# Kernel tuning notes

Measured on AMD Instinct MI355X. Metric: run time of the kernel, lower is better.

Reference implementation:

```python
import jax, jax.numpy as jnp
import numpy as np

B, T, D = 2, 2048, 1024
QH, KVH = 16, 4
HD = D // QH          # 64
G = QH // KVH         # group size 4
SCALE = HD ** -0.5


def _rope_rotate(x):
    # interleaved rotation: (x1, x2) -> (-x2, x1)
    x1 = x[..., ::2]
    x2 = x[..., 1::2]
    return jnp.stack((-x2, x1), axis=-1).reshape(x.shape)


def setup_inputs() -> dict:
    key = jax.random.key(0)
    k0, k1, k2, k3 = jax.random.split(key, 4)
    x = jax.random.normal(k0, (B, T, D), dtype=jnp.float32)
    # proper RoPE tables, shape [T, HD], each frequency repeated for the interleaved pair
    inv_freq = 1.0 / (10000.0 ** (np.arange(0, HD, 2, dtype=np.float32) / HD))
    freqs = np.arange(T, dtype=np.float32)[:, None] * inv_freq[None, :]   # [T, HD/2]
    freqs = np.repeat(freqs, 2, axis=-1)                                   # [T, HD]
    cos = jnp.asarray(np.cos(freqs), dtype=jnp.float32)
    sin = jnp.asarray(np.sin(freqs), dtype=jnp.float32)
    # glorot-uniform weights stored torch-style as [out, in]
    def glorot(k, out_d, in_d):
        lim = float(np.sqrt(6.0 / (in_d + out_d)))
        return jax.random.uniform(k, (out_d, in_d), jnp.float32, -lim, lim)
    Wq = glorot(k1, D, D)
    Wkv = glorot(k2, 2 * KVH * HD, D)
    Wo = glorot(k3, D, D)
    return {"x": x, "cos": cos, "sin": sin, "Wq": Wq, "Wkv": Wkv, "Wo": Wo}


def reference(x, cos, sin, Wq, Wkv, Wo):
    # projections (torch Linear: y = x @ W.T)
    q = (x @ Wq.T).reshape(B, T, QH, HD).transpose(0, 2, 1, 3)        # [B,QH,T,HD]
    kv = (x @ Wkv.T).reshape(B, T, KVH, 2, HD)
    k = kv[..., 0, :].transpose(0, 2, 1, 3)                            # [B,KVH,T,HD]
    v = kv[..., 1, :].transpose(0, 2, 1, 3)                            # [B,KVH,T,HD]
    # inline RoPE (cos/sin broadcast over batch & heads)
    q = q * cos + _rope_rotate(q) * sin
    k = k * cos + _rope_rotate(k) * sin
    # GQA via broadcast instead of repeat_interleave (same math)
    qg = q.reshape(B, KVH, G, T, HD)
    scores = jnp.einsum('bkgtd,bksd->bkgts', qg, k) * SCALE            # [B,KVH,G,T,T]
    attn = jax.nn.softmax(scores, axis=-1)  # dropout is identity in eval
    out = jnp.einsum('bkgts,bksd->bkgtd', attn, v)                     # [B,KVH,G,T,HD]
    out = out.reshape(B, QH, T, HD).transpose(0, 2, 1, 3).reshape(B, T, D)
    return out @ Wo.T
```

## Files before the change

kernel.cpp:

```cpp
#include <hip/hip_runtime.h>


typedef __bf16 bf16x8 __attribute__((ext_vector_type(8)));
typedef float f32x4 __attribute__((ext_vector_type(4)));
typedef float f32x16 __attribute__((ext_vector_type(16)));
typedef int i32x4 __attribute__((ext_vector_type(4)));
typedef unsigned short ushort4v __attribute__((ext_vector_type(4)));
typedef unsigned short ushort8v __attribute__((ext_vector_type(8)));
typedef unsigned short u16;
typedef unsigned int u32;

#define DEVINL __device__ __forceinline__

DEVINL float bf2f(u16 u) {
  unsigned int x = ((unsigned int)u) << 16;
  return __builtin_bit_cast(float, x);
}
DEVINL u16 f2bf(float f) {
  unsigned int x = __builtin_bit_cast(unsigned int, f);
  x += 0x7fffu + ((x >> 16) & 1u);
  return (u16)(x >> 16);
}
DEVINL float exp2r(float x) {
  float r;
  asm("v_exp_f32 %0, %1" : "=v"(r) : "v"(x));
  return r;
}

constexpr int Bb = 2, Tt = 2048, Dd = 1024, QH = 16, KVH = 4, HD = 64;
constexpr float SCALE_L2E = 0.125f * 1.44269504088896340736f;
constexpr int KVSZ = 131072;

__global__ void cvt_all(const float* __restrict__ x, const float* __restrict__ Wq,
                        const float* __restrict__ Wkv, const float* __restrict__ Wo,
                        u16* __restrict__ xb, u16* __restrict__ wqkv,
                        u16* __restrict__ wob) {
  int i = blockIdx.x * 256 + threadIdx.x;
  const float* src;
  u16* dst;
  if (i < 1048576) {
    src = x; dst = xb;
  } else if (i < 1310720) {
    src = Wq - (size_t)1048576 * 4; dst = wqkv - (size_t)1048576 * 4;
  } else if (i < 1441792) {
    src = Wkv - (size_t)1310720 * 4; dst = wqkv + (size_t)1024 * 1024 - (size_t)1310720 * 4;
  } else {
    src = Wo - (size_t)1441792 * 4; dst = wob - (size_t)1441792 * 4;
  }
  float4 v = reinterpret_cast<const float4*>(src)[i];
  ushort4v o = {f2bf(v.x), f2bf(v.y), f2bf(v.z), f2bf(v.w)};
  *reinterpret_cast<ushort4v*>(dst + (size_t)i * 4) = o;
}

template <bool OUT_F32>
__global__ __launch_bounds__(256) void gemm_bt(const u16* __restrict__ A,
                                               const u16* __restrict__ Bw,
                                               void* __restrict__ Cout, int M, int N, int K) {
  __shared__ alignas(16) u16 lA[128 * 64];
  __shared__ alignas(16) u16 lB[128 * 64];
  const int tid = threadIdx.x;
  const int w = tid >> 6, lane = tid & 63;
  const int r16 = lane & 15, g4 = lane >> 4;
  const int row0 = blockIdx.y * 128, col0 = blockIdx.x * 128;
  const int sr = tid >> 3, sc = tid & 7;
  const int NT = K >> 6;

  bf16x8 ra[4], rb[4];
  f32x4 acc[4][4];
#pragma unroll
  for (int i = 0; i < 4; ++i)
#pragma unroll
    for (int j = 0; j < 4; ++j) acc[i][j] = f32x4{0.f, 0.f, 0.f, 0.f};

  const int wm = (w >> 1) * 64, wn = (w & 1) * 64;

#pragma unroll
  for (int i = 0; i < 4; ++i) {
    int r = i * 32 + sr;
    ra[i] = *reinterpret_cast<const bf16x8*>(A + (size_t)(row0 + r) * K + sc * 8);
    rb[i] = *reinterpret_cast<const bf16x8*>(Bw + (size_t)(col0 + r) * K + sc * 8);
  }

  for (int kt = 0; kt < NT; ++kt) {
    __syncthreads();
#pragma unroll
    for (int i = 0; i < 4; ++i) {
      int r = i * 32 + sr;
      int c = (sc ^ (r & 7)) * 8;
      *reinterpret_cast<bf16x8*>(&lA[r * 64 + c]) = ra[i];
      *reinterpret_cast<bf16x8*>(&lB[r * 64 + c]) = rb[i];
    }
    __syncthreads();
    if (kt + 1 < NT) {
      int k0 = (kt + 1) << 6;
#pragma unroll
      for (int i = 0; i < 4; ++i) {
        int r = i * 32 + sr;
        ra[i] = *reinterpret_cast<const bf16x8*>(A + (size_t)(row0 + r) * K + k0 + sc * 8);
        rb[i] = *reinterpret_cast<const bf16x8*>(Bw + (size_t)(col0 + r) * K + k0 + sc * 8);
      }
    }
#pragma unroll
    for (int kk = 0; kk < 2; ++kk) {
      bf16x8 af[4], bfr[4];
#pragma unroll
      for (int mf = 0; mf < 4; ++mf) {
        int r = wm + mf * 16 + r16;
        int c = ((kk * 4 + g4) ^ (r & 7)) * 8;
        af[mf] = *reinterpret_cast<const bf16x8*>(&lA[r * 64 + c]);
      }
#pragma unroll
      for (int nf = 0; nf < 4; ++nf) {
        int r = wn + nf * 16 + r16;
        int c = ((kk * 4 + g4) ^ (r & 7)) * 8;
        bfr[nf] = *reinterpret_cast<const bf16x8*>(&lB[r * 64 + c]);
      }
#pragma unroll
      for (int mf = 0; mf < 4; ++mf)
#pragma unroll
        for (int nf = 0; nf < 4; ++nf)
          acc[mf][nf] =
              __builtin_amdgcn_mfma_f32_16x16x32_bf16(af[mf], bfr[nf], acc[mf][nf], 0, 0, 0);
    }
  }

#pragma unroll
  for (int mf = 0; mf < 4; ++mf)
#pragma unroll
    for (int nf = 0; nf < 4; ++nf)
#pragma unroll
      for (int r = 0; r < 4; ++r) {
        size_t row = (size_t)(row0 + wm + mf * 16 + g4 * 4 + r);
        size_t col = (size_t)(col0 + wn + nf * 16 + r16);
        float v = acc[mf][nf][r];
        if (OUT_F32)
          reinterpret_cast<float*>(Cout)[row * N + col] = v;
        else
          reinterpret_cast<u16*>(Cout)[row * N + col] = f2bf(v);
      }
}

__global__ void rope_scatter(const u16* __restrict__ P, const float* __restrict__ cosT,
                             const float* __restrict__ sinT, u16* __restrict__ Q,
                             u16* __restrict__ Kc) {
  int idx = blockIdx.x * 256 + threadIdx.x;
  if (idx >= (Bb * Tt) * 640) return;
  int row = idx / 640, p = idx - row * 640;
  int b = row >> 11, t = row & 2047;
  int n, d;
  u16* outp;
  float scl;
  if (p < 512) {
    n = p * 2;
    int h = n >> 6;
    d = n & 63;
    outp = Q + ((size_t)(b * QH + h) * Tt + t) * HD + d;
    scl = SCALE_L2E;
  } else {
    int r2 = p - 512;
    int kvh = r2 >> 5, dp = r2 & 31;
    d = dp * 2;
    n = 1024 + kvh * 128 + d;
    int bh = b * KVH + kvh;
    int kf = d >> 4, h8 = (d >> 3) & 1, j = d & 7;
    outp = Kc + (size_t)bh * KVSZ + ((t >> 5) * 4 + kf) * 512 + (h8 * 32 + (t & 31)) * 8 + j;
    scl = 1.0f;
  }
  unsigned int pv = *reinterpret_cast<const unsigned int*>(P + (size_t)row * 1536 + n);
  float v0 = bf2f((u16)(pv & 0xffffu)), v1 = bf2f((u16)(pv >> 16));
  float c = cosT[t * HD + d], s = sinT[t * HD + d];
  float o0 = (v0 * c - v1 * s) * scl;
  float o1 = (v1 * c + v0 * s) * scl;
  unsigned int ob = (unsigned int)f2bf(o0) | ((unsigned int)f2bf(o1) << 16);
  *reinterpret_cast<unsigned int*>(outp) = ob;
}

__global__ void v_transpose(const u16* __restrict__ P, u16* __restrict__ Vf) {
  __shared__ u16 tile[64][72];
  int bh = blockIdx.y;
  int b = bh >> 2, kvh = bh & 3;
  int t0 = blockIdx.x * 64;
  int tid = threadIdx.x;
  int colbase = 1024 + kvh * 128 + 64;
#pragma unroll
  for (int j = 0; j < 4; ++j) {
    int rr = j * 16 + (tid >> 4);
    int cc = (tid & 15) * 4;
    *reinterpret_cast<uint2*>(&tile[rr][cc]) =
        *reinterpret_cast<const uint2*>(P + (size_t)(b * Tt + t0 + rr) * 1536 + colbase + cc);
  }
  __syncthreads();
#pragma unroll
  for (int kk = 0; kk < 2; ++kk) {
    int CH = kk * 256 + tid;
    int df = CH >> 8, sbks = (CH >> 6) & 3, h8 = (CH >> 5) & 1, l = CH & 31;
    int d = df * 32 + l;
    int c = (sbks >> 1) * 4 + (sbks & 1) * 2 + h8;
    ushort8v v;
#pragma unroll
    for (int j = 0; j < 8; ++j) v[j] = tile[c * 8 + j][d];
    u16* dst = Vf + (size_t)bh * KVSZ + (((t0 >> 6) * 2 + df) * 4 + sbks) * 512 +
               (h8 * 32 + l) * 8;
    *reinterpret_cast<ushort8v*>(dst) = v;
  }
}

__global__ __launch_bounds__(512, 4) void attn_fwd7(const u16* __restrict__ Q,
                                                    const u16* __restrict__ Kf,
                                                    const u16* __restrict__ Vf,
                                                    u16* __restrict__ Oa) {
  __shared__ alignas(16) float cmb[2][32][66];
  __shared__ alignas(16) u16 ot[2][32][72];
  const int tid = threadIdx.x;
  const int w = tid >> 6, lane = tid & 63;
  const int qsub = w & 1, spl = w >> 1;
  const int l31 = lane & 31, hi = lane >> 5;

  const int fid = blockIdx.x;
  const int xcd = fid & 7, idx = fid >> 3;
  const int b = xcd >> 2, kvh = xcd & 3;
  const int g = idx & 3, qblk = idx >> 2;
  const int h = kvh * 4 + g;
  const int t0 = qblk * 64 + qsub * 32;

  const u16* Qh = Q + ((size_t)(b * QH + h) * Tt + t0 + l31) * HD + hi * 8;
  const u16* Kp = Kf + (size_t)(b * KVH + kvh) * KVSZ + lane * 8 + (size_t)spl * 32768;
  const u16* Vp = Vf + (size_t)(b * KVH + kvh) * KVSZ + lane * 8 + (size_t)spl * 32768;

  bf16x8 qf[4];
#pragma unroll
  for (int kf = 0; kf < 4; ++kf)
    qf[kf] = *reinterpret_cast<const bf16x8*>(Qh + kf * 16);

  f32x16 oacc[2];
#pragma unroll
  for (int df = 0; df < 2; ++df)
#pragma unroll
    for (int r = 0; r < 16; ++r) oacc[df][r] = 0.f;
  float lp = 0.f;

  for (int it = 0; it < 8; ++it, Kp += 4096, Vp += 4096) {
    f32x16 sacc[2];
#pragma unroll
    for (int sb = 0; sb < 2; ++sb) {
      bf16x8 kfr[4];
#pragma unroll
      for (int kf = 0; kf < 4; ++kf)
        kfr[kf] = *reinterpret_cast<const bf16x8*>(Kp + sb * 2048 + kf * 512);
#pragma unroll
      for (int r = 0; r < 16; ++r) sacc[sb][r] = 0.f;
      __builtin_amdgcn_s_setprio(1);
#pragma unroll
      for (int kf = 0; kf < 4; ++kf)
        sacc[sb] = __builtin_amdgcn_mfma_f32_32x32x16_bf16(kfr[kf], qf[kf], sacc[sb], 0, 0, 0);
      __builtin_amdgcn_s_setprio(0);
    }

    float a0 = 0.f, a1 = 0.f, a2 = 0.f, a3 = 0.f;
#pragma unroll
    for (int sb = 0; sb < 2; ++sb)
#pragma unroll
      for (int r = 0; r < 16; r += 4) {
        float e0 = exp2r(sacc[sb][r]);
        float e1 = exp2r(sacc[sb][r + 1]);
        float e2 = exp2r(sacc[sb][r + 2]);
        float e3 = exp2r(sacc[sb][r + 3]);
        sacc[sb][r] = e0; sacc[sb][r + 1] = e1; sacc[sb][r + 2] = e2; sacc[sb][r + 3] = e3;
        a0 += e0; a1 += e1; a2 += e2; a3 += e3;
      }
    lp += (a0 + a1) + (a2 + a3);

    bf16x8 pf[2][2];
#pragma unroll
    for (int sb = 0; sb < 2; ++sb) {
      u32 pw[8];
#pragma unroll
      for (int r2 = 0; r2 < 8; ++r2) {
        u32 o;
        asm("v_cvt_pk_bf16_f32 %0, %1, %2"
            : "=v"(o)
            : "v"(sacc[sb][2 * r2]), "v"(sacc[sb][2 * r2 + 1]));
        pw[r2] = o;
      }
      u32 fw[2][4];
#pragma unroll
      for (int pp = 0; pp < 4; ++pp) {
        int ks = pp >> 1, o = pp & 1;
        u32 a = pw[ks * 4 + o], bq = pw[ks * 4 + o + 2];
        asm("v_permlane32_swap_b32 %0, %1" : "+v"(a), "+v"(bq));
        fw[ks][o] = a;
        fw[ks][o + 2] = bq;
      }
#pragma unroll
      for (int ks = 0; ks < 2; ++ks) {
        i32x4 iv = {(int)fw[ks][0], (int)fw[ks][1], (int)fw[ks][2], (int)fw[ks][3]};
        pf[sb][ks] = __builtin_bit_cast(bf16x8, iv);
      }
    }

    bf16x8 vf[2][2][2];
#pragma unroll
    for (int df = 0; df < 2; ++df)
#pragma unroll
      for (int sb = 0; sb < 2; ++sb)
#pragma unroll
        for (int ks = 0; ks < 2; ++ks)
          vf[df][sb][ks] =
              *reinterpret_cast<const bf16x8*>(Vp + (size_t)(df * 4 + sb * 2 + ks) * 512);

    __builtin_amdgcn_s_setprio(1);
#pragma unroll
    for (int df = 0; df < 2; ++df)
#pragma unroll
      for (int sb = 0; sb < 2; ++sb)
#pragma unroll
        for (int ks = 0; ks < 2; ++ks)
          oacc[df] =
              __builtin_amdgcn_mfma_f32_32x32x16_bf16(vf[df][sb][ks], pf[sb][ks], oacc[df], 0, 0, 0);
    __builtin_amdgcn_s_setprio(0);
  }

  lp += __shfl_xor(lp, 32);

  for (int src = 1; src < 4; ++src) {
    if (spl == src) {
      float* cb = &cmb[qsub][l31][0];
#pragma unroll
      for (int df = 0; df < 2; ++df)
#pragma unroll
        for (int r = 0; r < 16; ++r) {
          int d = df * 32 + (r & 3) + 8 * (r >> 2) + 4 * hi;
          cb[d] = oacc[df][r];
        }
      if (hi == 0) cb[64] = lp;
    }
    __syncthreads();
    if (spl == 0) {
      const float* cb = &cmb[qsub][l31][0];
      lp += cb[64];
#pragma unroll
      for (int df = 0; df < 2; ++df)
#pragma unroll
        for (int r = 0; r < 16; ++r) {
          int d = df * 32 + (r & 3) + 8 * (r >> 2) + 4 * hi;
          oacc[df][r] += cb[d];
        }
    }
    __syncthreads();
  }

  if (spl == 0) {
    float linv = 1.0f / lp;
#pragma unroll
    for (int df = 0; df < 2; ++df)
#pragma unroll
      for (int r = 0; r < 16; ++r) {
        int d = df * 32 + (r & 3) + 8 * (r >> 2) + 4 * hi;
        ot[qsub][l31][d] = f2bf(oacc[df][r] * linv);
      }
  }
  __syncthreads();
  if (spl == 0) {
    int tr = lane >> 1, dblk = (lane & 1) * 32;
    u16* gdst = Oa + ((size_t)(b * Tt + t0 + tr)) * Dd + h * HD + dblk;
#pragma unroll
    for (int c = 0; c < 4; ++c) {
      ushort8v vv = *reinterpret_cast<const ushort8v*>(&ot[qsub][tr][dblk + c * 8]);
      *reinterpret_cast<ushort8v*>(gdst + c * 8) = vv;
    }
  }
}

extern "C" void kernel_launch(void* const* d_in, const int* in_sizes, int n_in, void* d_out,
                              int out_size, void* d_ws, size_t ws_size, hipStream_t stream) {
  (void)in_sizes; (void)n_in; (void)out_size; (void)ws_size;
  const float* x = (const float*)d_in[0];
  const float* cosT = (const float*)d_in[1];
  const float* sinT = (const float*)d_in[2];
  const float* Wq = (const float*)d_in[3];
  const float* Wkv = (const float*)d_in[4];
  const float* Wo = (const float*)d_in[5];

  char* p = (char*)d_ws;
  u16* xb = (u16*)p;   p += (size_t)4096 * 1024 * 2;
  u16* wqkv = (u16*)p; p += (size_t)1536 * 1024 * 2;
  u16* wob = (u16*)p;  p += (size_t)1024 * 1024 * 2;
  u16* Pbuf = (u16*)p; p += (size_t)4096 * 1536 * 2;
  u16* Qb = (u16*)p;   p += (size_t)Bb * QH * Tt * HD * 2;
  u16* Kbuf = (u16*)p; p += (size_t)Bb * KVH * Tt * HD * 2;
  u16* Vfb = (u16*)p;  p += (size_t)Bb * KVH * HD * Tt * 2;
  u16* Ob = Pbuf;

  cvt_all<<<6656, 256, 0, stream>>>(x, Wq, Wkv, Wo, xb, wqkv, wob);
  gemm_bt<false><<<dim3(12, 32), 256, 0, stream>>>(xb, wqkv, Pbuf, 4096, 1536, 1024);
  rope_scatter<<<10240, 256, 0, stream>>>(Pbuf, cosT, sinT, Qb, Kbuf);
  v_transpose<<<dim3(32, 8), 256, 0, stream>>>(Pbuf, Vfb);
  attn_fwd7<<<1024, 512, 0, stream>>>(Qb, Kbuf, Vfb, Ob);
  gemm_bt<true><<<dim3(8, 32), 256, 0, stream>>>(Ob, wob, d_out, 4096, 1024, 1024);
}
```

Before: 109.9 us.

## Merge rope and V-transpose kernels, hoist K/V loads, narrow output GEMM tiles

Fuses the rope_scatter and v_transpose kernels into one launch that picks its role from the block index, saving a kernel launch. In the attention loop, all K fragments are loaded before the QK MFMAs and the V loads move ahead of the softmax, so memory latency overlaps with compute. The GEMM gains a template parameter for N-tile width, and the output projection uses 64-wide tiles to double its block count (512 blocks) for better CU occupancy. The costs are higher register pressure in attention and less data reuse per block in the narrower GEMM.

```diff
diff --git a/kernel.cpp b/kernel.cpp
--- a/kernel.cpp
+++ b/kernel.cpp
@@ -52,32 +52,36 @@
   *reinterpret_cast<ushort4v*>(dst + (size_t)i * 4) = o;
 }
 
-template <bool OUT_F32>
+template <bool OUT_F32, int BNF>
 __global__ __launch_bounds__(256) void gemm_bt(const u16* __restrict__ A,
                                                const u16* __restrict__ Bw,
                                                void* __restrict__ Cout, int M, int N, int K) {
   __shared__ alignas(16) u16 lA[128 * 64];
-  __shared__ alignas(16) u16 lB[128 * 64];
+  __shared__ alignas(16) u16 lB[BNF * 32 * 64];
   const int tid = threadIdx.x;
   const int w = tid >> 6, lane = tid & 63;
   const int r16 = lane & 15, g4 = lane >> 4;
-  const int row0 = blockIdx.y * 128, col0 = blockIdx.x * 128;
+  const int row0 = blockIdx.y * 128, col0 = blockIdx.x * (BNF * 32);
   const int sr = tid >> 3, sc = tid & 7;
   const int NT = K >> 6;
 
-  bf16x8 ra[4], rb[4];
-  f32x4 acc[4][4];
+  bf16x8 ra[4], rb[BNF];
+  f32x4 acc[4][BNF];
 #pragma unroll
   for (int i = 0; i < 4; ++i)
 #pragma unroll
-    for (int j = 0; j < 4; ++j) acc[i][j] = f32x4{0.f, 0.f, 0.f, 0.f};
-
-  const int wm = (w >> 1) * 64, wn = (w & 1) * 64;
+    for (int j = 0; j < BNF; ++j) acc[i][j] = f32x4{0.f, 0.f, 0.f, 0.f};
+
+  const int wm = (w >> 1) * 64, wn = (w & 1) * (BNF * 8);
 
 #pragma unroll
   for (int i = 0; i < 4; ++i) {
     int r = i * 32 + sr;
     ra[i] = *reinterpret_cast<const bf16x8*>(A + (size_t)(row0 + r) * K + sc * 8);
+  }
+#pragma unroll
+  for (int i = 0; i < BNF; ++i) {
+    int r = i * 32 + sr;
     rb[i] = *reinterpret_cast<const bf16x8*>(Bw + (size_t)(col0 + r) * K + sc * 8);
   }
 
@@ -88,6 +92,11 @@
       int r = i * 32 + sr;
       int c = (sc ^ (r & 7)) * 8;
       *reinterpret_cast<bf16x8*>(&lA[r * 64 + c]) = ra[i];
+    }
+#pragma unroll
+    for (int i = 0; i < BNF; ++i) {
+      int r = i * 32 + sr;
+      int c = (sc ^ (r & 7)) * 8;
       *reinterpret_cast<bf16x8*>(&lB[r * 64 + c]) = rb[i];
     }
     __syncthreads();
@@ -97,12 +106,16 @@
       for (int i = 0; i < 4; ++i) {
         int r = i * 32 + sr;
         ra[i] = *reinterpret_cast<const bf16x8*>(A + (size_t)(row0 + r) * K + k0 + sc * 8);
+      }
+#pragma unroll
+      for (int i = 0; i < BNF; ++i) {
+        int r = i * 32 + sr;
         rb[i] = *reinterpret_cast<const bf16x8*>(Bw + (size_t)(col0 + r) * K + k0 + sc * 8);
       }
     }
 #pragma unroll
     for (int kk = 0; kk < 2; ++kk) {
-      bf16x8 af[4], bfr[4];
+      bf16x8 af[4], bfr[BNF];
 #pragma unroll
       for (int mf = 0; mf < 4; ++mf) {
         int r = wm + mf * 16 + r16;
@@ -110,15 +123,15 @@
         af[mf] = *reinterpret_cast<const bf16x8*>(&lA[r * 64 + c]);
       }
 #pragma unroll
-      for (int nf = 0; nf < 4; ++nf) {
-        int r = wn + nf * 16 + r16;
+      for (int nf = 0; nf < BNF; ++nf) {
+        int r = wn * 2 + nf * 16 + r16;
         int c = ((kk * 4 + g4) ^ (r & 7)) * 8;
         bfr[nf] = *reinterpret_cast<const bf16x8*>(&lB[r * 64 + c]);
       }
 #pragma unroll
       for (int mf = 0; mf < 4; ++mf)
 #pragma unroll
-        for (int nf = 0; nf < 4; ++nf)
+        for (int nf = 0; nf < BNF; ++nf)
           acc[mf][nf] =
               __builtin_amdgcn_mfma_f32_16x16x32_bf16(af[mf], bfr[nf], acc[mf][nf], 0, 0, 0);
     }
@@ -127,11 +140,11 @@
 #pragma unroll
   for (int mf = 0; mf < 4; ++mf)
 #pragma unroll
-    for (int nf = 0; nf < 4; ++nf)
+    for (int nf = 0; nf < BNF; ++nf)
 #pragma unroll
       for (int r = 0; r < 4; ++r) {
         size_t row = (size_t)(row0 + wm + mf * 16 + g4 * 4 + r);
-        size_t col = (size_t)(col0 + wn + nf * 16 + r16);
+        size_t col = (size_t)(col0 + wn * 2 + nf * 16 + r16);
         float v = acc[mf][nf][r];
         if (OUT_F32)
           reinterpret_cast<float*>(Cout)[row * N + col] = v;
@@ -140,72 +153,73 @@
       }
 }
 
-__global__ void rope_scatter(const u16* __restrict__ P, const float* __restrict__ cosT,
-                             const float* __restrict__ sinT, u16* __restrict__ Q,
-                             u16* __restrict__ Kc) {
-  int idx = blockIdx.x * 256 + threadIdx.x;
-  if (idx >= (Bb * Tt) * 640) return;
-  int row = idx / 640, p = idx - row * 640;
-  int b = row >> 11, t = row & 2047;
-  int n, d;
-  u16* outp;
-  float scl;
-  if (p < 512) {
-    n = p * 2;
-    int h = n >> 6;
-    d = n & 63;
-    outp = Q + ((size_t)(b * QH + h) * Tt + t) * HD + d;
-    scl = SCALE_L2E;
+__global__ void rope_vt(const u16* __restrict__ P, const float* __restrict__ cosT,
+                        const float* __restrict__ sinT, u16* __restrict__ Q,
+                        u16* __restrict__ Kc, u16* __restrict__ Vf) {
+  __shared__ u16 tile[64][72];
+  const int bid = blockIdx.x;
+  const int tid = threadIdx.x;
+  if (bid < 10240) {
+    int idx = bid * 256 + tid;
+    int row = idx / 640, p = idx - row * 640;
+    int b = row >> 11, t = row & 2047;
+    int n, d;
+    u16* outp;
+    float scl;
+    if (p < 512) {
+      n = p * 2;
+      int h = n >> 6;
+      d = n & 63;
+      outp = Q + ((size_t)(b * QH + h) * Tt + t) * HD + d;
+      scl = SCALE_L2E;
+    } else {
+      int r2 = p - 512;
+      int kvh = r2 >> 5, dp = r2 & 31;
+      d = dp * 2;
+      n = 1024 + kvh * 128 + d;
+      int bh = b * KVH + kvh;
+      int kf = d >> 4, h8 = (d >> 3) & 1, j = d & 7;
+      outp = Kc + (size_t)bh * KVSZ + ((t >> 5) * 4 + kf) * 512 + (h8 * 32 + (t & 31)) * 8 + j;
+      scl = 1.0f;
+    }
+    unsigned int pv = *reinterpret_cast<const unsigned int*>(P + (size_t)row * 1536 + n);
+    float v0 = bf2f((u16)(pv & 0xffffu)), v1 = bf2f((u16)(pv >> 16));
+    float c = cosT[t * HD + d], s = sinT[t * HD + d];
+    float o0 = (v0 * c - v1 * s) * scl;
+    float o1 = (v1 * c + v0 * s) * scl;
+    unsigned int ob = (unsigned int)f2bf(o0) | ((unsigned int)f2bf(o1) << 16);
+    *reinterpret_cast<unsigned int*>(outp) = ob;
   } else {
-    int r2 = p - 512;
-    int kvh = r2 >> 5, dp = r2 & 31;
-    d = dp * 2;
-    n = 1024 + kvh * 128 + d;
-    int bh = b * KVH + kvh;
-    int kf = d >> 4, h8 = (d >> 3) & 1, j = d & 7;
-    outp = Kc + (size_t)bh * KVSZ + ((t >> 5) * 4 + kf) * 512 + (h8 * 32 + (t & 31)) * 8 + j;
-    scl = 1.0f;
-  }
-  unsigned int pv = *reinterpret_cast<const unsigned int*>(P + (size_t)row * 1536 + n);
-  float v0 = bf2f((u16)(pv & 0xffffu)), v1 = bf2f((u16)(pv >> 16));
-  float c = cosT[t * HD + d], s = sinT[t * HD + d];
-  float o0 = (v0 * c - v1 * s) * scl;
-  float o1 = (v1 * c + v0 * s) * scl;
-  unsigned int ob = (unsigned int)f2bf(o0) | ((unsigned int)f2bf(o1) << 16);
-  *reinterpret_cast<unsigned int*>(outp) = ob;
-}
-
-__global__ void v_transpose(const u16* __restrict__ P, u16* __restrict__ Vf) {
-  __shared__ u16 tile[64][72];
-  int bh = blockIdx.y;
-  int b = bh >> 2, kvh = bh & 3;
-  int t0 = blockIdx.x * 64;
-  int tid = threadIdx.x;
-  int colbase = 1024 + kvh * 128 + 64;
-#pragma unroll
-  for (int j = 0; j < 4; ++j) {
-    int rr = j * 16 + (tid >> 4);
-    int cc = (tid & 15) * 4;
-    *reinterpret_cast<uint2*>(&tile[rr][cc]) =
-        *reinterpret_cast<const uint2*>(P + (size_t)(b * Tt + t0 + rr) * 1536 + colbase + cc);
-  }
-  __syncthreads();
-#pragma unroll
-  for (int kk = 0; kk < 2; ++kk) {
-    int CH = kk * 256 + tid;
-    int df = CH >> 8, sbks = (CH >> 6) & 3, h8 = (CH >> 5) & 1, l = CH & 31;
-    int d = df * 32 + l;
-    int c = (sbks >> 1) * 4 + (sbks & 1) * 2 + h8;
-    ushort8v v;
-#pragma unroll
-    for (int j = 0; j < 8; ++j) v[j] = tile[c * 8 + j][d];
-    u16* dst = Vf + (size_t)bh * KVSZ + (((t0 >> 6) * 2 + df) * 4 + sbks) * 512 +
-               (h8 * 32 + l) * 8;
-    *reinterpret_cast<ushort8v*>(dst) = v;
-  }
-}
-
-__global__ __launch_bounds__(512, 4) void attn_fwd7(const u16* __restrict__ Q,
+    int rem = bid - 10240;
+    int bh = rem >> 5, tt = rem & 31;
+    int b = bh >> 2, kvh = bh & 3;
+    int t0 = tt * 64;
+    int colbase = 1024 + kvh * 128 + 64;
+#pragma unroll
+    for (int j = 0; j < 4; ++j) {
+      int rr = j * 16 + (tid >> 4);
+      int cc = (tid & 15) * 4;
+      *reinterpret_cast<uint2*>(&tile[rr][cc]) =
+          *reinterpret_cast<const uint2*>(P + (size_t)(b * Tt + t0 + rr) * 1536 + colbase + cc);
+    }
+    __syncthreads();
+#pragma unroll
+    for (int kk = 0; kk < 2; ++kk) {
+      int CH = kk * 256 + tid;
+      int df = CH >> 8, sbks = (CH >> 6) & 3, h8 = (CH >> 5) & 1, l = CH & 31;
+      int d = df * 32 + l;
+      int c = (sbks >> 1) * 4 + (sbks & 1) * 2 + h8;
+      ushort8v v;
+#pragma unroll
+      for (int j = 0; j < 8; ++j) v[j] = tile[c * 8 + j][d];
+      u16* dst = Vf + (size_t)bh * KVSZ + (((t0 >> 6) * 2 + df) * 4 + sbks) * 512 +
+                 (h8 * 32 + l) * 8;
+      *reinterpret_cast<ushort8v*>(dst) = v;
+    }
+  }
+}
+
+__global__ __launch_bounds__(512, 4) void attn_fwd9(const u16* __restrict__ Q,
                                                     const u16* __restrict__ Kf,
                                                     const u16* __restrict__ Vf,
                                                     u16* __restrict__ Oa) {
@@ -240,21 +254,35 @@
   float lp = 0.f;
 
   for (int it = 0; it < 8; ++it, Kp += 4096, Vp += 4096) {
+    bf16x8 kfr[2][4];
+#pragma unroll
+    for (int sb = 0; sb < 2; ++sb)
+#pragma unroll
+      for (int kf = 0; kf < 4; ++kf)
+        kfr[sb][kf] = *reinterpret_cast<const bf16x8*>(Kp + sb * 2048 + kf * 512);
+
     f32x16 sacc[2];
 #pragma unroll
-    for (int sb = 0; sb < 2; ++sb) {
-      bf16x8 kfr[4];
+    for (int sb = 0; sb < 2; ++sb)
+#pragma unroll
+      for (int r = 0; r < 16; ++r) sacc[sb][r] = 0.f;
+    __builtin_amdgcn_s_setprio(1);
+#pragma unroll
+    for (int sb = 0; sb < 2; ++sb)
 #pragma unroll
       for (int kf = 0; kf < 4; ++kf)
-        kfr[kf] = *reinterpret_cast<const bf16x8*>(Kp + sb * 2048 + kf * 512);
-#pragma unroll
-      for (int r = 0; r < 16; ++r) sacc[sb][r] = 0.f;
-      __builtin_amdgcn_s_setprio(1);
-#pragma unroll
-      for (int kf = 0; kf < 4; ++kf)
-        sacc[sb] = __builtin_amdgcn_mfma_f32_32x32x16_bf16(kfr[kf], qf[kf], sacc[sb], 0, 0, 0);
-      __builtin_amdgcn_s_setprio(0);
-    }
+        sacc[sb] = __builtin_amdgcn_mfma_f32_32x32x16_bf16(kfr[sb][kf], qf[kf], sacc[sb], 0, 0, 0);
+    __builtin_amdgcn_s_setprio(0);
+
+    bf16x8 vf[2][2][2];
+#pragma unroll
+    for (int df = 0; df < 2; ++df)
+#pragma unroll
+      for (int sb = 0; sb < 2; ++sb)
+#pragma unroll
+        for (int ks = 0; ks < 2; ++ks)
+          vf[df][sb][ks] =
+              *reinterpret_cast<const bf16x8*>(Vp + (size_t)(df * 4 + sb * 2 + ks) * 512);
 
     float a0 = 0.f, a1 = 0.f, a2 = 0.f, a3 = 0.f;
 #pragma unroll
@@ -297,16 +325,6 @@
         pf[sb][ks] = __builtin_bit_cast(bf16x8, iv);
       }
     }
-
-    bf16x8 vf[2][2][2];
-#pragma unroll
-    for (int df = 0; df < 2; ++df)
-#pragma unroll
-      for (int sb = 0; sb < 2; ++sb)
-#pragma unroll
-        for (int ks = 0; ks < 2; ++ks)
-          vf[df][sb][ks] =
-              *reinterpret_cast<const bf16x8*>(Vp + (size_t)(df * 4 + sb * 2 + ks) * 512);
 
     __builtin_amdgcn_s_setprio(1);
 #pragma unroll
@@ -392,9 +410,8 @@
   u16* Ob = Pbuf;
 
   cvt_all<<<6656, 256, 0, stream>>>(x, Wq, Wkv, Wo, xb, wqkv, wob);
-  gemm_bt<false><<<dim3(12, 32), 256, 0, stream>>>(xb, wqkv, Pbuf, 4096, 1536, 1024);
-  rope_scatter<<<10240, 256, 0, stream>>>(Pbuf, cosT, sinT, Qb, Kbuf);
-  v_transpose<<<dim3(32, 8), 256, 0, stream>>>(Pbuf, Vfb);
-  attn_fwd7<<<1024, 512, 0, stream>>>(Qb, Kbuf, Vfb, Ob);
-  gemm_bt<true><<<dim3(8, 32), 256, 0, stream>>>(Ob, wob, d_out, 4096, 1024, 1024);
-}
+  gemm_bt<false, 4><<<dim3(12, 32), 256, 0, stream>>>(xb, wqkv, Pbuf, 4096, 1536, 1024);
+  rope_vt<<<10496, 256, 0, stream>>>(Pbuf, cosT, sinT, Qb, Kbuf, Vfb);
+  attn_fwd9<<<1024, 512, 0, stream>>>(Qb, Kbuf, Vfb, Ob);
+  gemm_bt<true, 2><<<dim3(16, 32), 256, 0, stream>>>(Ob, wob, d_out, 4096, 1024, 1024);
+}
```

After: 107.4 us. -2.3%, faster.
